# Optimization experiments

Hardware: AMD Instinct MI355X
Metric: run time of the kernel (lower is better)

The kernel has to match this reference:

```python
import jax, jax.numpy as jnp
import numpy as np

CAPACITY = (0.1, 0.15, 0.25, 0.5)  # must sum to 1.0
B, N, D = 8, 8192, 1024
E = len(CAPACITY)


def setup_inputs() -> dict:
    key = jax.random.key(0)
    k1, k2 = jax.random.split(key)
    x = jax.random.normal(k1, (B, N, D), dtype=jnp.float32)
    # router weight init: uniform(-0.02, 0.02), bias zeros (matches _init_weights)
    W = jax.random.uniform(k2, (E, D), minval=-0.02, maxval=0.02, dtype=jnp.float32)
    b = jnp.zeros((E,), dtype=jnp.float32)
    return {"input_tokens": x, "W": W, "b": b}


def _route(probs):
    """Capacity-constrained expert-preferred assignment.

    probs: [B, N, E] softmax router probabilities.
    Returns token_mask [B, N] int32: expert id per token.
    """
    Bn, Nn, En = probs.shape
    k = jnp.floor(jnp.asarray(CAPACITY, probs.dtype) * Nn).astype(jnp.int32)  # [E]
    token_mask = jnp.full((Bn, Nn), -1, dtype=jnp.int32)
    unassigned = jnp.ones((Bn, Nn), dtype=bool)
    rows = jnp.arange(Bn)[:, None]
    pos = jnp.arange(Nn)[None, :]
    neg_inf = jnp.asarray(-jnp.inf, probs.dtype)
    # iterate experts from largest index (biggest expert preference) down to 0
    for j in range(En - 1, -1, -1):
        r_j = jnp.where(unassigned, probs[:, :, j], neg_inf)          # [B, N]
        sorted_idx = jnp.argsort(-r_j, axis=1)                        # descending
        num_unassigned = unassigned.sum(axis=1).astype(jnp.int32)     # [B]
        k_i = jnp.minimum(k[j], num_unassigned)                        # [B]
        topk = pos < k_i[:, None]                                      # [B, N] over sorted order
        # scatter sorted-order selection back to token order
        assigned_this = jnp.zeros((Bn, Nn), bool).at[rows, sorted_idx].set(topk)
        token_mask = jnp.where(assigned_this, j, token_mask)
        unassigned = unassigned & ~assigned_this
    return jnp.where(token_mask == -1, 0, token_mask)


def reference(input_tokens, W, b):
    # thin router GEMM: [B,N,D] x [E,D] -> [B,N,E]
    logits = jnp.einsum('bnd,ed->bne', input_tokens, W) + b
    probs = jax.nn.softmax(logits, axis=-1)
    token_mask = _route(probs)  # [B, N] int32
    expert_probs = jnp.take_along_axis(probs, token_mask[..., None], axis=2)[..., 0]
    return token_mask, expert_probs
```

## Files before the change

### kernel.cpp

```cpp
#include <hip/hip_runtime.h>
#include <math.h>

namespace {

constexpr int B = 8;
constexpr int N = 8192;
constexpr int D = 1024;
constexpr int E = 4;
constexpr int BN = B * N;

__device__ __forceinline__ unsigned int orderkey(float p) {
    return __float_as_uint(p) | 0x80000000u;
}

__device__ __forceinline__ double fast_exp64(double x) {
    const double L2E    = 1.4426950408889634074;
    const double LN2_HI = 6.93147180369123816490e-01;
    const double LN2_LO = 1.90821492927058770002e-10;
    const double nd = rint(x * L2E);
    double r = fma(-nd, LN2_HI, x);
    r = fma(-nd, LN2_LO, r);
    double p = 1.0 / 479001600.0;
    p = fma(p, r, 1.0 / 39916800.0);
    p = fma(p, r, 1.0 / 3628800.0);
    p = fma(p, r, 1.0 / 362880.0);
    p = fma(p, r, 1.0 / 40320.0);
    p = fma(p, r, 1.0 / 5040.0);
    p = fma(p, r, 1.0 / 720.0);
    p = fma(p, r, 1.0 / 120.0);
    p = fma(p, r, 1.0 / 24.0);
    p = fma(p, r, 1.0 / 6.0);
    p = fma(p, r, 0.5);
    p = fma(p, r, 1.0);
    p = fma(p, r, 1.0);
    const long long sc = ((long long)(1023 + (int)nd)) << 52;
    return p * __longlong_as_double(sc);
}

__global__ __launch_bounds__(256) void probs_kernel(
    const float* __restrict__ x,
    const float* __restrict__ W,
    const float* __restrict__ bias,
    float* __restrict__ probs_t)
{
    __shared__ float4 s_W4[E][D / 4];
    __shared__ double s_l[64][4];

    {
        const float4* W4 = reinterpret_cast<const float4*>(W);
        for (int i = threadIdx.x; i < E * D / 4; i += 256)
            s_W4[i >> 8][i & 255] = W4[i];
    }
    __syncthreads();

    const int lane = threadIdx.x & 63;
    const int wv = threadIdx.x >> 6;
    const int tok0 = blockIdx.x * 64 + wv * 16;
    const int j = ((lane & 1) << 1) | ((lane >> 1) & 1);

    const float4* x4 = reinterpret_cast<const float4*>(x);

    for (int k = 0; k < 16; ++k) {
        const float4* xv = x4 + (size_t)(tok0 + k) * (D / 4);
        const float4 c0 = xv[lane];
        const float4 c1 = xv[lane + 64];
        const float4 c2 = xv[lane + 128];
        const float4 c3 = xv[lane + 192];

        double a0 = 0.0, a1 = 0.0, a2 = 0.0, a3 = 0.0;
#define CHUNK(XC, CI)                                                          \
        {                                                                      \
            const int idx = lane + 64 * (CI);                                  \
            const double xx = (double)(XC).x, xy = (double)(XC).y;             \
            const double xz = (double)(XC).z, xw = (double)(XC).w;             \
            const float4 w0 = s_W4[0][idx];                                    \
            a0 = fma(xx, (double)w0.x, a0); a0 = fma(xy, (double)w0.y, a0);    \
            a0 = fma(xz, (double)w0.z, a0); a0 = fma(xw, (double)w0.w, a0);    \
            const float4 w1 = s_W4[1][idx];                                    \
            a1 = fma(xx, (double)w1.x, a1); a1 = fma(xy, (double)w1.y, a1);    \
            a1 = fma(xz, (double)w1.z, a1); a1 = fma(xw, (double)w1.w, a1);    \
            const float4 w2 = s_W4[2][idx];                                    \
            a2 = fma(xx, (double)w2.x, a2); a2 = fma(xy, (double)w2.y, a2);    \
            a2 = fma(xz, (double)w2.z, a2); a2 = fma(xw, (double)w2.w, a2);    \
            const float4 w3 = s_W4[3][idx];                                    \
            a3 = fma(xx, (double)w3.x, a3); a3 = fma(xy, (double)w3.y, a3);    \
            a3 = fma(xz, (double)w3.z, a3); a3 = fma(xw, (double)w3.w, a3);    \
        }
        CHUNK(c0, 0) CHUNK(c1, 1) CHUNK(c2, 2) CHUNK(c3, 3)
#undef CHUNK

        {
            const double v = (lane & 1) ? a0 : a2;
            const double w = (lane & 1) ? a1 : a3;
            const double sv = __shfl_xor(v, 1, 64);
            const double sw = __shfl_xor(w, 1, 64);
            const double s0 = (lane & 1) ? (a2 + sv) : (a0 + sv);
            const double s1 = (lane & 1) ? (a3 + sw) : (a1 + sw);
            const double tt = (lane & 2) ? s0 : s1;
            const double st = __shfl_xor(tt, 2, 64);
            double s = (lane & 2) ? (s1 + st) : (s0 + st);
            s += __shfl_xor(s, 4, 64);
            s += __shfl_xor(s, 8, 64);
            s += __shfl_xor(s, 16, 64);
            s += __shfl_xor(s, 32, 64);
            if (lane < 4) s_l[wv * 16 + k][j] = s;
        }
    }
    __syncthreads();

    {
        const int tok = threadIdx.x >> 2;
        const int e = threadIdx.x & 3;
        const double l0 = s_l[tok][0] + (double)bias[0];
        const double l1 = s_l[tok][1] + (double)bias[1];
        const double l2 = s_l[tok][2] + (double)bias[2];
        const double l3 = s_l[tok][3] + (double)bias[3];
        const double m = fmax(fmax(l0, l1), fmax(l2, l3));
        const double le = (e == 0) ? l0 : (e == 1) ? l1 : (e == 2) ? l2 : l3;
        const double ex = fast_exp64(le - m);
        double Z = ex + __shfl_xor(ex, 1, 64);
        Z += __shfl_xor(Z, 2, 64);
        const double p = ex / Z;
        const int token = blockIdx.x * 64 + tok;
        const int brow = token >> 13;
        const int n = token & (N - 1);
        probs_t[((size_t)brow * E + e) * N + n] = (float)p;
    }
}

__global__ __launch_bounds__(1024) void route_kernel(
    const float* __restrict__ probs_t,
    float* __restrict__ out)
{
    constexpr int TPB = 1024;
    constexpr int ITEMS = N / TPB;
    constexpr int NBKT = 4096;
    constexpr int CMAX = 64;

    __shared__ unsigned short s_bkt4[E][N];
    __shared__ unsigned char s_exp[N];
    __shared__ unsigned int s_hist[NBKT];
    __shared__ unsigned int s_cand[CMAX];
    __shared__ unsigned int s_ckey[CMAX];
    __shared__ unsigned int s_wsum[32];
    __shared__ unsigned int s_sel[3];

    const int b = blockIdx.x;
    const int t = threadIdx.x;
    const int lane = t & 63;
    const int wv = t >> 6;

    for (int u = 0; u < ITEMS; ++u) s_exp[u * TPB + t] = 255;
#pragma unroll
    for (int e = 0; e < E; ++e) {
        const float* pe = probs_t + ((size_t)b * E + e) * N;
        for (int u = 0; u < ITEMS; ++u) {
            const int i = u * TPB + t;
            const float p = pe[i];
            int bk = (int)(p * 4096.0f);
            bk = bk > 4095 ? 4095 : (bk < 0 ? 0 : bk);
            s_bkt4[e][i] = (unsigned short)bk;
        }
    }

    const int kcap[E] = {819, 1228, 2048, 4096};
    int nun = N;

    for (int j = E - 1; j >= 0; --j) {
        const bool first = (j == E - 1);
        const int kk = min(kcap[j], nun);
        const float* pj = probs_t + ((size_t)b * E + j) * N;

        for (int u = 0; u < NBKT / TPB; ++u) s_hist[u * TPB + t] = 0;
        if (t == 0) s_sel[2] = 0;
        __syncthreads();

        for (int u = 0; u < ITEMS; ++u) {
            const int i = u * TPB + t;
            if (first || s_exp[i] == 255) atomicAdd(&s_hist[s_bkt4[j][i]], 1u);
        }
        __syncthreads();

        const unsigned int h0 = s_hist[4 * t], h1 = s_hist[4 * t + 1];
        const unsigned int h2 = s_hist[4 * t + 2], h3 = s_hist[4 * t + 3];
        const unsigned int lsum = h0 + h1 + h2 + h3;
        unsigned int sfx = lsum;
#pragma unroll
        for (int off = 1; off < 64; off <<= 1) {
            const unsigned int vv = __shfl_down(sfx, off, 64);
            if (lane + off < 64) sfx += vv;
        }
        if (lane == 0) s_wsum[wv] = sfx;
        __syncthreads();
        if (t < 16) {
            unsigned int acc = 0;
            for (int w2 = t + 1; w2 < 16; ++w2) acc += s_wsum[w2];
            s_wsum[16 + t] = acc;
        }
        __syncthreads();
        {
            unsigned int run = (sfx - lsum) + s_wsum[16 + wv];
            const unsigned int hh[4] = {h0, h1, h2, h3};
#pragma unroll
            for (int bi = 3; bi >= 0; --bi) {
                const unsigned int h = hh[bi];
                if (run < (unsigned)kk && run + h >= (unsigned)kk) {
                    s_sel[0] = (unsigned)(4 * t + bi);
                    s_sel[1] = (unsigned)kk - run;
                }
                run += h;
            }
        }
        __syncthreads();
        const int Bstar = (int)s_sel[0];
        const unsigned int rem = s_sel[1];

        for (int u = 0; u < ITEMS; ++u) {
            const int i = u * TPB + t;
            if (!first && s_exp[i] != 255) continue;
            const int bk = s_bkt4[j][i];
            if (bk > Bstar) {
                s_exp[i] = (unsigned char)j;
            } else if (bk == Bstar) {
                const unsigned int pos = atomicAdd(&s_sel[2], 1u);
                if (pos < CMAX) { s_cand[pos] = (unsigned int)i; s_ckey[pos] = orderkey(pj[i]); }
            }
        }
        __syncthreads();
        const unsigned int c = s_sel[2];

        if (rem == c) {
            for (int u = 0; u < ITEMS; ++u) {
                const int i = u * TPB + t;
                if ((first || s_exp[i] == 255) && s_bkt4[j][i] == Bstar)
                    s_exp[i] = (unsigned char)j;
            }
            __syncthreads();
        } else if (c <= CMAX) {
            if (wv == 0) {
                unsigned int key = 0u, idx = 0xFFFFFFFFu;
                if (lane < (int)c) { key = s_ckey[lane]; idx = s_cand[lane]; }
                unsigned long long v = ((unsigned long long)(~key) << 32) | idx;
                for (int k2 = 2; k2 <= 64; k2 <<= 1) {
                    for (int jj = k2 >> 1; jj >= 1; jj >>= 1) {
                        const unsigned long long pv = __shfl_xor(v, jj, 64);
                        const bool up = ((lane & k2) == 0);
                        const bool lower = ((lane & jj) == 0);
                        if (lower == up) v = (v < pv) ? v : pv;
                        else             v = (v > pv) ? v : pv;
                    }
                }
                if (lane < (int)rem) {
                    const unsigned int tok = (unsigned int)(v & 0xFFFFFFFFu);
                    s_exp[tok] = (unsigned char)j;
                }
            }
            __syncthreads();
        } else {
            unsigned int prefix = 0, remR = rem;
            for (int shift = 24; shift >= 0; shift -= 8) {
                if (t < 256) s_hist[t] = 0;
                __syncthreads();
                for (int u = 0; u < ITEMS; ++u) {
                    const int i = t * ITEMS + u;
                    if (s_exp[i] != 255) continue;
                    const unsigned int key = orderkey(pj[i]);
                    if (shift == 24 || (key >> (shift + 8)) == prefix)
                        atomicAdd(&s_hist[(key >> shift) & 255u], 1u);
                }
                __syncthreads();
                if (wv == 0) {
                    const unsigned int g0 = s_hist[4 * lane], g1 = s_hist[4 * lane + 1];
                    const unsigned int g2 = s_hist[4 * lane + 2], g3 = s_hist[4 * lane + 3];
                    const unsigned int ls = g0 + g1 + g2 + g3;
                    unsigned int sx = ls;
#pragma unroll
                    for (int off = 1; off < 64; off <<= 1) {
                        const unsigned int vv = __shfl_down(sx, off, 64);
                        if (lane + off < 64) sx += vv;
                    }
                    unsigned int rr = sx - ls;
                    const unsigned int gg[4] = {g0, g1, g2, g3};
#pragma unroll
                    for (int bi = 3; bi >= 0; --bi) {
                        const unsigned int h = gg[bi];
                        if (rr < remR && rr + h >= remR) {
                            s_sel[0] = (unsigned)(4 * lane + bi);
                            s_sel[1] = remR - rr;
                        }
                        rr += h;
                    }
                }
                __syncthreads();
                prefix = (prefix << 8) | s_sel[0];
                remR = s_sel[1];
            }
            const unsigned int T = prefix;
            unsigned int local = 0;
            for (int u = 0; u < ITEMS; ++u) {
                const int i = t * ITEMS + u;
                if (s_exp[i] == 255 && orderkey(pj[i]) == T) ++local;
            }
            unsigned int inc = local;
#pragma unroll
            for (int off = 1; off < 64; off <<= 1) {
                const unsigned int vv = __shfl_up(inc, off, 64);
                if (lane >= off) inc += vv;
            }
            if (lane == 63) s_wsum[wv] = inc;
            __syncthreads();
            if (t < 16) {
                unsigned int a2 = 0;
                for (int w2 = 0; w2 < t; ++w2) a2 += s_wsum[w2];
                s_wsum[16 + t] = a2;
            }
            __syncthreads();
            unsigned int taken = (inc - local) + s_wsum[16 + wv];
            for (int u = 0; u < ITEMS; ++u) {
                const int i = t * ITEMS + u;
                if (s_exp[i] != 255) continue;
                const unsigned int key = orderkey(pj[i]);
                if (key > T) {
                    s_exp[i] = (unsigned char)j;
                } else if (key == T) {
                    if (taken < remR) s_exp[i] = (unsigned char)j;
                    ++taken;
                }
            }
            __syncthreads();
        }
        nun -= kk;
    }

    float* out_mask = out;
    float* out_p = out + (size_t)BN;
    for (int u = 0; u < ITEMS; ++u) {
        const int i = u * TPB + t;
        int e = s_exp[i];
        if (e == 255) e = 0;
        out_mask[(size_t)b * N + i] = (float)e;
        out_p[(size_t)b * N + i] = probs_t[((size_t)b * E + e) * N + i];
    }
}

}

extern "C" void kernel_launch(void* const* d_in, const int* in_sizes, int n_in,
                              void* d_out, int out_size, void* d_ws, size_t ws_size,
                              hipStream_t stream) {
    const float* x = (const float*)d_in[0];
    const float* W = (const float*)d_in[1];
    const float* bias = (const float*)d_in[2];
    float* out = (float*)d_out;
    float* probs_t = (float*)d_ws;

    probs_kernel<<<BN / 64, 256, 0, stream>>>(x, W, bias, probs_t);
    route_kernel<<<B, 1024, 0, stream>>>(probs_t, out);
}
```

Before: 79.24 us.

## Double-buffer x tiles into LDS via async global_load_lds and pre-convert W to double

The router GEMM kernel now stages groups of four tokens' x rows into a double-buffered LDS tile using the async global-to-LDS load builtin, prefetching the next group while computing the current one. W is converted to double once and stored in LDS, which removes the per-FMA float-to-double conversions. Token ordering changes so each iteration covers four tokens across the four waves. Costs: a block-wide barrier every iteration and more LDS use, which may reduce occupancy.

```diff
diff --git a/kernel.cpp b/kernel.cpp
--- a/kernel.cpp
+++ b/kernel.cpp
@@ -1,5 +1,6 @@
 #include <hip/hip_runtime.h>
 #include <math.h>
+#include <stdint.h>
 
 namespace {
 
@@ -8,6 +9,9 @@
 constexpr int D = 1024;
 constexpr int E = 4;
 constexpr int BN = B * N;
+
+typedef __attribute__((address_space(3))) uint32_t lds_u32;
+typedef __attribute__((address_space(1))) const uint32_t glb_u32;
 
 __device__ __forceinline__ unsigned int orderkey(float p) {
     return __float_as_uint(p) | 0x80000000u;
@@ -43,29 +47,53 @@
     const float* __restrict__ bias,
     float* __restrict__ probs_t)
 {
-    __shared__ float4 s_W4[E][D / 4];
+    __shared__ double2 s_WA[E][D / 4];
+    __shared__ double2 s_WB[E][D / 4];
+    __shared__ float s_x[2][4 * D];
     __shared__ double s_l[64][4];
+
+    const int lane = threadIdx.x & 63;
+    const int wv = threadIdx.x >> 6;
+    const int tok0 = blockIdx.x * 64;
+    const int j = ((lane & 1) << 1) | ((lane >> 1) & 1);
 
     {
         const float4* W4 = reinterpret_cast<const float4*>(W);
-        for (int i = threadIdx.x; i < E * D / 4; i += 256)
-            s_W4[i >> 8][i & 255] = W4[i];
-    }
+        for (int i = threadIdx.x; i < E * D / 4; i += 256) {
+            const int e = i >> 8, q = i & 255;
+            const float4 w = W4[i];
+            s_WA[e][q] = make_double2((double)w.x, (double)w.y);
+            s_WB[e][q] = make_double2((double)w.z, (double)w.w);
+        }
+    }
+
+    const char* xbase = (const char*)(x + (size_t)tok0 * D);
+
+    auto stage = [&](int buf, int g) {
+        const char* src = xbase + (size_t)g * (4 * D * 4);
+        char* dst = (char*)&s_x[buf][0];
+#pragma unroll
+        for (int s = 0; s < 4; ++s) {
+            const int base_chunk = s * 256 + wv * 64;
+            __builtin_amdgcn_global_load_lds(
+                (glb_u32*)(src + (size_t)(base_chunk + lane) * 16),
+                (lds_u32*)(dst + (size_t)base_chunk * 16),
+                16, 0, 0);
+        }
+    };
+
+    stage(0, 0);
     __syncthreads();
 
-    const int lane = threadIdx.x & 63;
-    const int wv = threadIdx.x >> 6;
-    const int tok0 = blockIdx.x * 64 + wv * 16;
-    const int j = ((lane & 1) << 1) | ((lane >> 1) & 1);
-
-    const float4* x4 = reinterpret_cast<const float4*>(x);
-
-    for (int k = 0; k < 16; ++k) {
-        const float4* xv = x4 + (size_t)(tok0 + k) * (D / 4);
-        const float4 c0 = xv[lane];
-        const float4 c1 = xv[lane + 64];
-        const float4 c2 = xv[lane + 128];
-        const float4 c3 = xv[lane + 192];
+    for (int g = 0; g < 16; ++g) {
+        const int buf = g & 1;
+        if (g < 15) stage(buf ^ 1, g + 1);
+
+        const float4* xt = (const float4*)&s_x[buf][wv * D];
+        const float4 c0 = xt[lane];
+        const float4 c1 = xt[lane + 64];
+        const float4 c2 = xt[lane + 128];
+        const float4 c3 = xt[lane + 192];
 
         double a0 = 0.0, a1 = 0.0, a2 = 0.0, a3 = 0.0;
 #define CHUNK(XC, CI)                                                          \
@@ -73,18 +101,26 @@
             const int idx = lane + 64 * (CI);                                  \
             const double xx = (double)(XC).x, xy = (double)(XC).y;             \
             const double xz = (double)(XC).z, xw = (double)(XC).w;             \
-            const float4 w0 = s_W4[0][idx];                                    \
-            a0 = fma(xx, (double)w0.x, a0); a0 = fma(xy, (double)w0.y, a0);    \
-            a0 = fma(xz, (double)w0.z, a0); a0 = fma(xw, (double)w0.w, a0);    \
-            const float4 w1 = s_W4[1][idx];                                    \
-            a1 = fma(xx, (double)w1.x, a1); a1 = fma(xy, (double)w1.y, a1);    \
-            a1 = fma(xz, (double)w1.z, a1); a1 = fma(xw, (double)w1.w, a1);    \
-            const float4 w2 = s_W4[2][idx];                                    \
-            a2 = fma(xx, (double)w2.x, a2); a2 = fma(xy, (double)w2.y, a2);    \
-            a2 = fma(xz, (double)w2.z, a2); a2 = fma(xw, (double)w2.w, a2);    \
-            const float4 w3 = s_W4[3][idx];                                    \
-            a3 = fma(xx, (double)w3.x, a3); a3 = fma(xy, (double)w3.y, a3);    \
-            a3 = fma(xz, (double)w3.z, a3); a3 = fma(xw, (double)w3.w, a3);    \
+            {                                                                  \
+                const double2 wA = s_WA[0][idx], wB = s_WB[0][idx];            \
+                a0 = fma(xx, wA.x, a0); a0 = fma(xy, wA.y, a0);                \
+                a0 = fma(xz, wB.x, a0); a0 = fma(xw, wB.y, a0);                \
+            }                                                                  \
+            {                                                                  \
+                const double2 wA = s_WA[1][idx], wB = s_WB[1][idx];            \
+                a1 = fma(xx, wA.x, a1); a1 = fma(xy, wA.y, a1);                \
+                a1 = fma(xz, wB.x, a1); a1 = fma(xw, wB.y, a1);                \
+            }                                                                  \
+            {                                                                  \
+                const double2 wA = s_WA[2][idx], wB = s_WB[2][idx];            \
+                a2 = fma(xx, wA.x, a2); a2 = fma(xy, wA.y, a2);                \
+                a2 = fma(xz, wB.x, a2); a2 = fma(xw, wB.y, a2);                \
+            }                                                                  \
+            {                                                                  \
+                const double2 wA = s_WA[3][idx], wB = s_WB[3][idx];            \
+                a3 = fma(xx, wA.x, a3); a3 = fma(xy, wA.y, a3);                \
+                a3 = fma(xz, wB.x, a3); a3 = fma(xw, wB.y, a3);                \
+            }                                                                  \
         }
         CHUNK(c0, 0) CHUNK(c1, 1) CHUNK(c2, 2) CHUNK(c3, 3)
 #undef CHUNK
@@ -103,10 +139,11 @@
             s += __shfl_xor(s, 8, 64);
             s += __shfl_xor(s, 16, 64);
             s += __shfl_xor(s, 32, 64);
-            if (lane < 4) s_l[wv * 16 + k][j] = s;
-        }
-    }
-    __syncthreads();
+            if (lane < 4) s_l[4 * g + wv][j] = s;
+        }
+
+        __syncthreads();
+    }
 
     {
         const int tok = threadIdx.x >> 2;
@@ -121,7 +158,7 @@
         double Z = ex + __shfl_xor(ex, 1, 64);
         Z += __shfl_xor(Z, 2, 64);
         const double p = ex / Z;
-        const int token = blockIdx.x * 64 + tok;
+        const int token = tok0 + tok;
         const int brow = token >> 13;
         const int n = token & (N - 1);
         probs_t[((size_t)brow * E + e) * N + n] = (float)p;
```

After: 81.33 us. 2.6% more time.
